# Kernel tuning notes

Measured on AMD Instinct MI355X. Metric: run time of the kernel, lower is better.

## Reference

```python
import jax, jax.numpy as jnp
import numpy as np

D, H, B = 16, 1024, 2048  # input_size, hidden_size, batch
EPS = 1e-12


def _masks():
    # MADE degree assignment, order 'A' (natural order)
    deg_in = jnp.arange(1, D + 1)                # [D]
    deg_h = jnp.arange(H) % (D - 1) + 1          # [H]
    m0 = (deg_h[:, None] >= deg_in[None, :]).astype(jnp.float32)  # [H, D] input->hidden
    m1 = (deg_h[:, None] >= deg_h[None, :]).astype(jnp.float32)   # [H, H] hidden->hidden
    m2 = (deg_in[:, None] > deg_h[None, :]).astype(jnp.float32)   # [D, H] hidden->output
    return m0, m1, m2


def setup_inputs() -> dict:
    key = jax.random.key(0)
    ks = jax.random.split(key, 8)

    def lin(k, out_d, in_d):
        k1, k2, k3 = jax.random.split(k, 3)
        v = jax.random.normal(k1, (out_d, in_d), jnp.float32)
        g = jax.random.uniform(k2, (out_d,), jnp.float32, 0.1, 0.2)  # small gain keeps logstd stable over D iters
        b = jax.random.normal(k3, (out_d,), jnp.float32) * 0.01
        return v, g, b

    inp = {"x": jax.random.normal(ks[0], (B, D), jnp.float32)}
    dims = [(H, D), (H, H), (D, H)]
    i = 1
    for n in ("mu", "lv"):
        for j, (o, ii) in enumerate(dims):
            v, g, b = lin(ks[i], o, ii)
            i += 1
            inp[f"{n}_v{j}"] = v
            inp[f"{n}_g{j}"] = g
            inp[f"{n}_b{j}"] = b
    return inp


def _wn(v, g, m):
    # weight-normalized masked linear weight: mask * g * v / ||v||
    return m * (g[:, None] * v / jnp.linalg.norm(v, axis=1, keepdims=True))


def _made(y, p):
    (w0, b0), (w1, b1), (w2, b2) = p
    h = jax.nn.elu(y @ w0.T + b0)   # [B, H]
    h = jax.nn.elu(h @ w1.T + b1)   # [B, H]
    return h @ w2.T + b2            # [B, D]


def reference(x, mu_v0, mu_g0, mu_b0, mu_v1, mu_g1, mu_b1, mu_v2, mu_g2, mu_b2,
              lv_v0, lv_g0, lv_b0, lv_v1, lv_g1, lv_b1, lv_v2, lv_g2, lv_b2):
    m0, m1, m2 = _masks()
    pm = ((_wn(mu_v0, mu_g0, m0), mu_b0), (_wn(mu_v1, mu_g1, m1), mu_b1), (_wn(mu_v2, mu_g2, m2), mu_b2))
    pl = ((_wn(lv_v0, lv_g0, m0), lv_b0), (_wn(lv_v1, lv_g1, m1), lv_b1), (_wn(lv_v2, lv_g2, m2), lv_b2))

    def step(carry, _):
        y, _ls = carry
        mu = _made(y, pm)
        logstd = _made(y, pl) * 0.5
        y_new = (x - mu) / (jnp.exp(logstd) + EPS)
        return (y_new, logstd), None

    init = (jnp.zeros_like(x), jnp.zeros_like(x))
    (y, logstd), _ = jax.lax.scan(step, init, None, length=D)
    return y, logstd.sum(axis=1)
```

## Files before the change

kernel.cpp:

```cpp
#include <hip/hip_runtime.h>
#include <cstdint>
#include <cstddef>


#define Dd 16
#define Hh 1024
#define Bb 2048
#define EPSV 1e-12f

typedef unsigned short u16;
typedef __attribute__((ext_vector_type(4))) float f32x4;
typedef __attribute__((ext_vector_type(8))) short s16x8;
typedef __attribute__((ext_vector_type(4))) u16 u16x4;
typedef __attribute__((ext_vector_type(8))) u16 u16x8;

__device__ __forceinline__ u16 f2bf(float f) {
  union { float f; unsigned u; } v; v.f = f;
  unsigned u = v.u;
  unsigned r = (u + 0x7fffu + ((u >> 16) & 1u)) >> 16;
  return (u16)r;
}
__device__ __forceinline__ float elu(float a) {
  return a > 0.f ? a : __expf(a) - 1.f;
}
__device__ __forceinline__ void barrier_lds() {
  asm volatile("s_waitcnt lgkmcnt(0)" ::: "memory");
  __builtin_amdgcn_s_barrier();
}

__device__ __forceinline__ int p_of(int i) {
  if (i < 276) { int g = i / 69, q = i - g * 69; return g + 15 * q; }
  int r = i - 276; int g = 4 + r / 68, q = r - (g - 4) * 68;
  return g + 15 * q;
}
__device__ __forceinline__ int g_of(int i) {
  return (i < 276) ? (i / 69) : (4 + (i - 276) / 68);
}
__device__ __forceinline__ int lb_of(int g) {
  return (g <= 4) ? 69 * g : 276 + 68 * (g - 4);
}
__device__ __forceinline__ int sz_of(int g) { return (g < 4) ? 69 : 68; }

#define W1P_NET (15 * 80 * 1024)
#define W2P_NET (15 * 16 * 104)
#define W0P_NET (15 * 80 * 32)

__global__ __launch_bounds__(256) void prep_all(
    const float* __restrict__ mu_v0, const float* __restrict__ mu_g0,
    const float* __restrict__ mu_b0,
    const float* __restrict__ mu_v1, const float* __restrict__ mu_g1,
    const float* __restrict__ mu_b1,
    const float* __restrict__ mu_v2, const float* __restrict__ mu_g2,
    const float* __restrict__ lv_v0, const float* __restrict__ lv_g0,
    const float* __restrict__ lv_b0,
    const float* __restrict__ lv_v1, const float* __restrict__ lv_g1,
    const float* __restrict__ lv_b1,
    const float* __restrict__ lv_v2, const float* __restrict__ lv_g2,
    u16* __restrict__ W1p, u16* __restrict__ W2p, u16* __restrict__ W0p,
    float* __restrict__ b1p, float* __restrict__ b0p) {
  int bid = blockIdx.x, tid = threadIdx.x;
  int l = tid & 63, w = tid >> 6;

  {
    int wid = bid * 4 + w;
    int net = wid / 1200, rem = wid % 1200;
    int g = rem / 80, u = rem % 80;
    u16* o = W1p + (size_t)wid * 1024;
    if (u < sz_of(g)) {
      int j = p_of(lb_of(g) + u);
      const float* v = (net ? lv_v1 : mu_v1) + (size_t)j * Hh;
      float val[4][4]; float ss = 0.f;
      for (int ii = 0; ii < 4; ++ii)
        for (int t = 0; t < 4; ++t) {
          int kp = ii * 256 + 4 * l + t;
          float xx = v[p_of(kp)];
          val[ii][t] = xx; ss += xx * xx;
        }
      for (int s = 32; s; s >>= 1) ss += __shfl_xor(ss, s);
      float sc = ((net ? lv_g1 : mu_g1)[j]) * rsqrtf(ss);
      for (int ii = 0; ii < 4; ++ii) {
        int k0 = ii * 256 + 4 * l;
        u16x4 wv;
        for (int t = 0; t < 4; ++t)
          wv[t] = f2bf((g >= g_of(k0 + t)) ? sc * val[ii][t] : 0.f);
        *(u16x4*)(o + k0) = wv;
      }
    } else {
      u16x4 z = {0, 0, 0, 0};
      for (int ii = 0; ii < 4; ++ii) *(u16x4*)(o + ii * 256 + 4 * l) = z;
    }
  }

  if (bid < 8) {
    int wid2 = bid * 4 + w;
    int nn = wid2 >> 4, oi = wid2 & 15;
    const float* v = (nn ? lv_v2 : mu_v2) + (size_t)oi * Hh;
    float ss = 0.f;
    for (int ii = 0; ii < 4; ++ii) {
      f32x4 vv = *(const f32x4*)(v + ii * 256 + 4 * l);
      ss += vv[0]*vv[0] + vv[1]*vv[1] + vv[2]*vv[2] + vv[3]*vv[3];
    }
    for (int s = 32; s; s >>= 1) ss += __shfl_xor(ss, s);
    float sc = ((nn ? lv_g2 : mu_g2)[oi]) * rsqrtf(ss);
    for (int e = l; e < 15 * 104; e += 64) {
      int g = e / 104, u = e % 104;
      float val = 0.f;
      if (u < sz_of(g) && oi > g) val = sc * v[p_of(lb_of(g) + u)];
      W2p[nn * W2P_NET + g * (16 * 104) + oi * 104 + u] = f2bf(val);
    }
  }

  if (bid >= 8 && bid < 18) {
    int idx = (bid - 8) * 256 + tid;
    if (idx < 2400) {
      int nn = idx / 1200, rem = idx % 1200;
      int g = rem / 80, u = rem % 80;
      u16* orow = W0p + nn * W0P_NET + g * (80 * 32) + u * 32;
      if (u < sz_of(g)) {
        int j = p_of(lb_of(g) + u);
        const float* v = (nn ? lv_v0 : mu_v0) + j * Dd;
        float vv[16]; float ss = 0.f;
        for (int k = 0; k < 16; ++k) { vv[k] = v[k]; ss += vv[k] * vv[k]; }
        float sc = ((nn ? lv_g0 : mu_g0)[j]) * rsqrtf(ss);
        for (int k = 0; k < 16; ++k)
          orow[k] = f2bf((g >= k) ? sc * vv[k] : 0.f);
        for (int k = 16; k < 32; ++k) orow[k] = 0;
        b0p[nn * 1200 + g * 80 + u] = (nn ? lv_b0 : mu_b0)[j];
        b1p[nn * 1200 + g * 80 + u] = (nn ? lv_b1 : mu_b1)[j];
      } else {
        for (int k = 0; k < 32; ++k) orow[k] = 0;
        b0p[nn * 1200 + g * 80 + u] = 0.f;
        b1p[nn * 1200 + g * 80 + u] = 0.f;
      }
    }
  }
}

__global__ __launch_bounds__(256) void prep_w1f(
    const u16* __restrict__ W1p, u16* __restrict__ W1f) {
  int t = blockIdx.x * 4 + (threadIdx.x >> 6);
  int l = threadIdx.x & 63;
  int net = t / 240, rem = t % 240;
  int g = rem >> 4, kt = rem & 15;
  if (kt >= ((lb_of(g + 1) + 63) >> 6)) return;
  const u16* src = W1p + (size_t)(net * 1200 + g * 80) * 1024;
  u16* dst = W1f + ((size_t)((net * 15 + g) * 16 + kt) * 10) * 512;
  for (int nf = 0; nf < 5; ++nf)
    for (int kk = 0; kk < 2; ++kk) {
      int u = nf * 16 + (l & 15);
      int k = kt * 64 + kk * 32 + ((l >> 4) << 3);
      u16x8 v = *(const u16x8*)(src + (size_t)u * 1024 + k);
      *(u16x8*)(dst + (size_t)(nf * 2 + kk) * 512 + l * 8) = v;
    }
}

#define LOADF(DST, BASE, KT)                                                \
  {                                                                         \
    const u16* fp_ = (BASE) + (size_t)(KT) * 5120;                          \
    _Pragma("unroll") for (int nf_ = 0; nf_ < 5; ++nf_)                     \
      _Pragma("unroll") for (int kk_ = 0; kk_ < 2; ++kk_)                   \
        DST[nf_][kk_] = *(const s16x8*)(fp_ + (nf_ * 2 + kk_) * 512);       \
  }
#define MFMAI(SLOT, KT)                                                     \
  {                                                                         \
    s16x8 a0_ = *(const s16x8*)(&h0L[net][lr][(KT) * 64 + lk * 8]);         \
    s16x8 a1_ = *(const s16x8*)(&h0L[net][lr][(KT) * 64 + 32 + lk * 8]);    \
    _Pragma("unroll") for (int nf_ = 0; nf_ < 5; ++nf_) {                   \
      hacc[nf_] = __builtin_amdgcn_mfma_f32_16x16x32_bf16(                  \
          a0_, SLOT[nf_][0], hacc[nf_], 0, 0, 0);                           \
      hacc[nf_] = __builtin_amdgcn_mfma_f32_16x16x32_bf16(                  \
          a1_, SLOT[nf_][1], hacc[nf_], 0, 0, 0);                           \
    }                                                                       \
  }

__global__ __launch_bounds__(512, 1) void afmade_main(
    const u16* __restrict__ W1f, const u16* __restrict__ W2p,
    const u16* __restrict__ W0p,
    const float* __restrict__ b1p, const float* __restrict__ b0p,
    const float* __restrict__ b2_mu, const float* __restrict__ b2_lv,
    const float* __restrict__ x, float* __restrict__ out) {
  __shared__ u16 h0L[2][16][1040];
  __shared__ float sPart[2][4][16][80];
  __shared__ u16 sH1[2][16][104];
  __shared__ u16 yb[16][40];
  __shared__ float sX[16][16];
  __shared__ float sB1L[2400];
  __shared__ float sB0L[2400];
  __shared__ float sB2[2][16];
  __shared__ float sLsum[16];

  const int tid = threadIdx.x;
  const int l = tid & 63, w = tid >> 6;
  const int net = w >> 2, kq = w & 3;
  const int lr = l & 15, lk = l >> 4;
  const int b0g = blockIdx.x * 16;

  {
    u16x8 z = {0, 0, 0, 0, 0, 0, 0, 0};
    for (int e = tid; e < 4160; e += 512) ((u16x8*)h0L)[e] = z;
    for (int e = tid; e < 416; e += 512) ((u16x8*)sH1)[e] = z;
    for (int e = tid; e < 80; e += 512) ((u16x8*)yb)[e] = z;
  }
  for (int e = tid; e < 256; e += 512)
    sX[e >> 4][e & 15] = x[(size_t)(b0g + (e >> 4)) * 16 + (e & 15)];
  for (int e = tid; e < 2400; e += 512) { sB1L[e] = b1p[e]; sB0L[e] = b0p[e]; }
  if (tid < 16) sB2[0][tid] = b2_mu[tid];
  else if (tid < 32) sB2[1][tid - 16] = b2_lv[tid - 16];
  else if (tid < 48) sLsum[tid - 32] = 0.f;
  f32x4 mlacc0 = {0.f, 0.f, 0.f, 0.f};
  f32x4 mlacc1 = {0.f, 0.f, 0.f, 0.f};

  s16x8 bfA[5][2], bfB[5][2], bfC[5][2];
  {
    const u16* base1 = W1f + ((size_t)((net * 15 + 0) * 16) * 10) * 512 +
                       (size_t)l * 8;
    if (kq < 2) LOADF(bfA, base1, kq);
  }
  __syncthreads();

  for (int s = 0; s < 16; ++s) {
    s16x8 w0pre0, w0pre1;
    if (s < 15) {
      const u16* W0g = W0p + net * W0P_NET + s * (80 * 32);
      w0pre0 = *(const s16x8*)(W0g + (kq * 16 + lr) * 32 + lk * 8);
      if (kq == 0)
        w0pre1 = *(const s16x8*)(W0g + (64 + lr) * 32 + lk * 8);
    }

    if (s > 0) {
      const int g = s - 1;
      const int ktn = (lb_of(s) + 63) >> 6;
      const int ktnN = (s < 15) ? ((lb_of(s + 1) + 63) >> 6) : 0;
      const u16* baseg = W1f + ((size_t)((net * 15 + g) * 16) * 10) * 512 +
                         (size_t)l * 8;
      const u16* basen = W1f + ((size_t)((net * 15 + s) * 16) * 10) * 512 +
                         (size_t)l * 8;
      s16x8 w2f[6];
      if (w == 0) {
#pragma unroll
        for (int c = 0; c < 3; ++c) {
          w2f[c] = *(const s16x8*)(W2p + g * (16 * 104) + lr * 104 +
                                   c * 32 + lk * 8);
          w2f[3 + c] = *(const s16x8*)(W2p + W2P_NET + g * (16 * 104) +
                                       lr * 104 + c * 32 + lk * 8);
        }
      }
      f32x4 hacc[5] = {};
      if (kq + 8 < ktn)  LOADF(bfC, baseg, kq + 8);
      if (kq < ktn)      MFMAI(bfA, kq);
      if (kq + 12 < ktn) LOADF(bfA, baseg, kq + 12);
      if (kq + 4 < ktn)  MFMAI(bfB, kq + 4);
      if (kq + 8 < ktn)  MFMAI(bfC, kq + 8);
      if (kq + 12 < ktn) MFMAI(bfA, kq + 12);
#pragma unroll
      for (int nf = 0; nf < 5; ++nf)
#pragma unroll
        for (int reg = 0; reg < 4; ++reg)
          sPart[net][kq][lk * 4 + reg][nf * 16 + lr] = hacc[nf][reg];
      if (s < 15) {
        if (kq < ktnN)     LOADF(bfA, basen, kq);
        if (kq + 4 < ktnN) LOADF(bfB, basen, kq + 4);
      }
      barrier_lds();
      {
        const int nn = tid >> 8;
        const int rr = (tid >> 4) & 15;
        const int u0 = tid & 15;
#pragma unroll
        for (int c = 0; c < 5; ++c) {
          int uu = c * 16 + u0;
          float v = sPart[nn][0][rr][uu] + sPart[nn][1][rr][uu] +
                    sPart[nn][2][rr][uu] + sPart[nn][3][rr][uu] +
                    sB1L[nn * 1200 + g * 80 + uu];
          sH1[nn][rr][uu] = f2bf(elu(v));
        }
      }
      barrier_lds();
      if (w == 0) {
#pragma unroll
        for (int c = 0; c < 3; ++c) {
          s16x8 a0 = *(const s16x8*)(&sH1[0][lr][c * 32 + lk * 8]);
          mlacc0 = __builtin_amdgcn_mfma_f32_16x16x32_bf16(
              a0, w2f[c], mlacc0, 0, 0, 0);
          s16x8 a1v = *(const s16x8*)(&sH1[1][lr][c * 32 + lk * 8]);
          mlacc1 = __builtin_amdgcn_mfma_f32_16x16x32_bf16(
              a1v, w2f[3 + c], mlacc1, 0, 0, 0);
        }
      }
    }
    if (w == 0 && lr == s) {
#pragma unroll
      for (int reg = 0; reg < 4; ++reg) {
        int r = lk * 4 + reg;
        float mu = mlacc0[reg] + sB2[0][s];
        float lv = mlacc1[reg] + sB2[1][s];
        float ls = 0.5f * lv;
        float yv = (sX[r][s] - mu) / (__expf(ls) + EPSV);
        out[(size_t)(b0g + r) * 16 + s] = yv;
        yb[r][s] = f2bf(yv);
        float ns = sLsum[r] + ls;
        sLsum[r] = ns;
        if (s == 15) out[Bb * 16 + b0g + r] = ns;
      }
    }
    barrier_lds();
    if (s < 15) {
      const int LbS = lb_of(s), szS = sz_of(s);
      s16x8 yfrag = *(const s16x8*)(&yb[lr][lk * 8]);
      {
        int nf = kq;
        int unit = nf * 16 + lr;
        f32x4 h = __builtin_amdgcn_mfma_f32_16x16x32_bf16(
            yfrag, w0pre0, (f32x4){0.f, 0.f, 0.f, 0.f}, 0, 0, 0);
        if (unit < szS) {
          float bias = sB0L[net * 1200 + s * 80 + unit];
#pragma unroll
          for (int reg = 0; reg < 4; ++reg)
            h0L[net][lk * 4 + reg][LbS + unit] = f2bf(elu(h[reg] + bias));
        }
      }
      if (kq == 0) {
        int unit = 64 + lr;
        f32x4 h = __builtin_amdgcn_mfma_f32_16x16x32_bf16(
            yfrag, w0pre1, (f32x4){0.f, 0.f, 0.f, 0.f}, 0, 0, 0);
        if (unit < szS) {
          float bias = sB0L[net * 1200 + s * 80 + unit];
#pragma unroll
          for (int reg = 0; reg < 4; ++reg)
            h0L[net][lk * 4 + reg][LbS + unit] = f2bf(elu(h[reg] + bias));
        }
      }
      barrier_lds();
    }
  }
}


extern "C" void kernel_launch(void* const* d_in, const int* in_sizes, int n_in,
                              void* d_out, int out_size, void* d_ws, size_t ws_size,
                              hipStream_t stream) {
  const float* x     = (const float*)d_in[0];
  const float* mu_v0 = (const float*)d_in[1];
  const float* mu_g0 = (const float*)d_in[2];
  const float* mu_b0 = (const float*)d_in[3];
  const float* mu_v1 = (const float*)d_in[4];
  const float* mu_g1 = (const float*)d_in[5];
  const float* mu_b1 = (const float*)d_in[6];
  const float* mu_v2 = (const float*)d_in[7];
  const float* mu_g2 = (const float*)d_in[8];
  const float* mu_b2 = (const float*)d_in[9];
  const float* lv_v0 = (const float*)d_in[10];
  const float* lv_g0 = (const float*)d_in[11];
  const float* lv_b0 = (const float*)d_in[12];
  const float* lv_v1 = (const float*)d_in[13];
  const float* lv_g1 = (const float*)d_in[14];
  const float* lv_b1 = (const float*)d_in[15];
  const float* lv_v2 = (const float*)d_in[16];
  const float* lv_g2 = (const float*)d_in[17];
  const float* lv_b2 = (const float*)d_in[18];

  char* ws = (char*)d_ws;
  u16*   W1p = (u16*)(ws);
  u16*   W2p = (u16*)(ws + 4915200);
  u16*   W0p = (u16*)(ws + 5015040);
  float* b1p = (float*)(ws + 5168640);
  float* b0p = (float*)(ws + 5178240);
  u16*   W1f = (u16*)(ws + 5187840);

  prep_all<<<600, 256, 0, stream>>>(
      mu_v0, mu_g0, mu_b0, mu_v1, mu_g1, mu_b1, mu_v2, mu_g2,
      lv_v0, lv_g0, lv_b0, lv_v1, lv_g1, lv_b1, lv_v2, lv_g2,
      W1p, W2p, W0p, b1p, b0p);
  prep_w1f<<<120, 256, 0, stream>>>(W1p, W1f);

  afmade_main<<<128, 512, 0, stream>>>(W1f, W2p, W0p, b1p, b0p,
                                       mu_b2, lv_b2, x, (float*)d_out);
}
```

Before: 81.43 us.

## Split batch into 8-row blocks of 4 waves to double grid size

Each block now handles 8 batch rows with 256 threads (2 waves per net splitting K) instead of 16 rows with 512 threads, and the grid goes from 128 to 256 blocks so more of the 256 CUs are used. The K-loop of the hidden-to-hidden MFMA is re-pipelined with two register buffers over 8 k-tiles per wave, and the partial-sum reduction drops from 4 to 2 slices. The 16-row MFMA tiles are now half wasted (rows duplicated via lr&7 and masked on store), and each block re-reads the full W1 weights, doubling global/L2 weight traffic.

```diff
diff --git a/kernel.cpp b/kernel.cpp
--- a/kernel.cpp
+++ b/kernel.cpp
@@ -163,8 +163,8 @@
   }
 #define MFMAI(SLOT, KT)                                                     \
   {                                                                         \
-    s16x8 a0_ = *(const s16x8*)(&h0L[net][lr][(KT) * 64 + lk * 8]);         \
-    s16x8 a1_ = *(const s16x8*)(&h0L[net][lr][(KT) * 64 + 32 + lk * 8]);    \
+    s16x8 a0_ = *(const s16x8*)(&h0L[net][lr & 7][(KT) * 64 + lk * 8]);     \
+    s16x8 a1_ = *(const s16x8*)(&h0L[net][lr & 7][(KT) * 64 + 32 + lk * 8]);\
     _Pragma("unroll") for (int nf_ = 0; nf_ < 5; ++nf_) {                   \
       hacc[nf_] = __builtin_amdgcn_mfma_f32_16x16x32_bf16(                  \
           a0_, SLOT[nf_][0], hacc[nf_], 0, 0, 0);                           \
@@ -173,44 +173,45 @@
     }                                                                       \
   }
 
-__global__ __launch_bounds__(512, 1) void afmade_main(
+__global__ __launch_bounds__(256, 2) void afmade_main(
     const u16* __restrict__ W1f, const u16* __restrict__ W2p,
     const u16* __restrict__ W0p,
     const float* __restrict__ b1p, const float* __restrict__ b0p,
     const float* __restrict__ b2_mu, const float* __restrict__ b2_lv,
     const float* __restrict__ x, float* __restrict__ out) {
-  __shared__ u16 h0L[2][16][1040];
-  __shared__ float sPart[2][4][16][80];
-  __shared__ u16 sH1[2][16][104];
-  __shared__ u16 yb[16][40];
-  __shared__ float sX[16][16];
+  __shared__ u16 h0L[2][8][1040];
+  __shared__ float sPart[2][2][8][80];
+  __shared__ u16 sH1[2][8][104];
+  __shared__ u16 yb[8][40];
+  __shared__ float sX[8][16];
   __shared__ float sB1L[2400];
   __shared__ float sB0L[2400];
   __shared__ float sB2[2][16];
-  __shared__ float sLsum[16];
+  __shared__ float sMLex[2][16];
+  __shared__ float sLsum[8];
 
   const int tid = threadIdx.x;
   const int l = tid & 63, w = tid >> 6;
-  const int net = w >> 2, kq = w & 3;
+  const int net = w >> 1, kq = w & 1;
   const int lr = l & 15, lk = l >> 4;
-  const int b0g = blockIdx.x * 16;
+  const int b0g = blockIdx.x * 8;
 
   {
     u16x8 z = {0, 0, 0, 0, 0, 0, 0, 0};
-    for (int e = tid; e < 4160; e += 512) ((u16x8*)h0L)[e] = z;
-    for (int e = tid; e < 416; e += 512) ((u16x8*)sH1)[e] = z;
-    for (int e = tid; e < 80; e += 512) ((u16x8*)yb)[e] = z;
-  }
-  for (int e = tid; e < 256; e += 512)
-    sX[e >> 4][e & 15] = x[(size_t)(b0g + (e >> 4)) * 16 + (e & 15)];
-  for (int e = tid; e < 2400; e += 512) { sB1L[e] = b1p[e]; sB0L[e] = b0p[e]; }
+    for (int e = tid; e < 2080; e += 256) ((u16x8*)h0L)[e] = z;
+    for (int e = tid; e < 208; e += 256) ((u16x8*)sH1)[e] = z;
+    if (tid < 40) ((u16x8*)yb)[tid] = z;
+  }
+  if (tid < 128) sX[tid >> 4][tid & 15] =
+      x[(size_t)(b0g + (tid >> 4)) * 16 + (tid & 15)];
+  for (int e = tid; e < 2400; e += 256) { sB1L[e] = b1p[e]; sB0L[e] = b0p[e]; }
   if (tid < 16) sB2[0][tid] = b2_mu[tid];
   else if (tid < 32) sB2[1][tid - 16] = b2_lv[tid - 16];
-  else if (tid < 48) sLsum[tid - 32] = 0.f;
+  else if (tid < 40) sLsum[tid - 32] = 0.f;
   f32x4 mlacc0 = {0.f, 0.f, 0.f, 0.f};
   f32x4 mlacc1 = {0.f, 0.f, 0.f, 0.f};
 
-  s16x8 bfA[5][2], bfB[5][2], bfC[5][2];
+  s16x8 bfA[5][2], bfB[5][2];
   {
     const u16* base1 = W1f + ((size_t)((net * 15 + 0) * 16) * 10) * 512 +
                        (size_t)l * 8;
@@ -219,12 +220,13 @@
   __syncthreads();
 
   for (int s = 0; s < 16; ++s) {
-    s16x8 w0pre0, w0pre1;
+    s16x8 w0pre0, w0pre1, w0pre2;
     if (s < 15) {
       const u16* W0g = W0p + net * W0P_NET + s * (80 * 32);
       w0pre0 = *(const s16x8*)(W0g + (kq * 16 + lr) * 32 + lk * 8);
+      w0pre1 = *(const s16x8*)(W0g + ((kq + 2) * 16 + lr) * 32 + lk * 8);
       if (kq == 0)
-        w0pre1 = *(const s16x8*)(W0g + (64 + lr) * 32 + lk * 8);
+        w0pre2 = *(const s16x8*)(W0g + (64 + lr) * 32 + lk * 8);
     }
 
     if (s > 0) {
@@ -246,31 +248,38 @@
         }
       }
       f32x4 hacc[5] = {};
-      if (kq + 8 < ktn)  LOADF(bfC, baseg, kq + 8);
+      if (kq + 2 < ktn)  LOADF(bfB, baseg, kq + 2);
       if (kq < ktn)      MFMAI(bfA, kq);
+      if (kq + 4 < ktn)  LOADF(bfA, baseg, kq + 4);
+      if (kq + 2 < ktn)  MFMAI(bfB, kq + 2);
+      if (kq + 6 < ktn)  LOADF(bfB, baseg, kq + 6);
+      if (kq + 4 < ktn)  MFMAI(bfA, kq + 4);
+      if (kq + 8 < ktn)  LOADF(bfA, baseg, kq + 8);
+      if (kq + 6 < ktn)  MFMAI(bfB, kq + 6);
+      if (kq + 10 < ktn) LOADF(bfB, baseg, kq + 10);
+      if (kq + 8 < ktn)  MFMAI(bfA, kq + 8);
       if (kq + 12 < ktn) LOADF(bfA, baseg, kq + 12);
-      if (kq + 4 < ktn)  MFMAI(bfB, kq + 4);
-      if (kq + 8 < ktn)  MFMAI(bfC, kq + 8);
+      if (kq + 10 < ktn) MFMAI(bfB, kq + 10);
+      if (kq + 14 < ktn) LOADF(bfB, baseg, kq + 14);
       if (kq + 12 < ktn) MFMAI(bfA, kq + 12);
+      if (kq + 14 < ktn) MFMAI(bfB, kq + 14);
 #pragma unroll
       for (int nf = 0; nf < 5; ++nf)
 #pragma unroll
-        for (int reg = 0; reg < 4; ++reg)
-          sPart[net][kq][lk * 4 + reg][nf * 16 + lr] = hacc[nf][reg];
-      if (s < 15) {
-        if (kq < ktnN)     LOADF(bfA, basen, kq);
-        if (kq + 4 < ktnN) LOADF(bfB, basen, kq + 4);
-      }
+        for (int reg = 0; reg < 4; ++reg) {
+          int row = lk * 4 + reg;
+          if (row < 8) sPart[net][kq][row][nf * 16 + lr] = hacc[nf][reg];
+        }
+      if (s < 15 && kq < ktnN) LOADF(bfA, basen, kq);
       barrier_lds();
       {
-        const int nn = tid >> 8;
-        const int rr = (tid >> 4) & 15;
+        const int nn = tid >> 7;
+        const int rr = (tid >> 4) & 7;
         const int u0 = tid & 15;
 #pragma unroll
         for (int c = 0; c < 5; ++c) {
           int uu = c * 16 + u0;
           float v = sPart[nn][0][rr][uu] + sPart[nn][1][rr][uu] +
-                    sPart[nn][2][rr][uu] + sPart[nn][3][rr][uu] +
                     sB1L[nn * 1200 + g * 80 + uu];
           sH1[nn][rr][uu] = f2bf(elu(v));
         }
@@ -279,10 +288,10 @@
       if (w == 0) {
 #pragma unroll
         for (int c = 0; c < 3; ++c) {
-          s16x8 a0 = *(const s16x8*)(&sH1[0][lr][c * 32 + lk * 8]);
+          s16x8 a0 = *(const s16x8*)(&sH1[0][lr & 7][c * 32 + lk * 8]);
           mlacc0 = __builtin_amdgcn_mfma_f32_16x16x32_bf16(
               a0, w2f[c], mlacc0, 0, 0, 0);
-          s16x8 a1v = *(const s16x8*)(&sH1[1][lr][c * 32 + lk * 8]);
+          s16x8 a1v = *(const s16x8*)(&sH1[1][lr & 7][c * 32 + lk * 8]);
           mlacc1 = __builtin_amdgcn_mfma_f32_16x16x32_bf16(
               a1v, w2f[3 + c], mlacc1, 0, 0, 0);
         }
@@ -292,42 +301,60 @@
 #pragma unroll
       for (int reg = 0; reg < 4; ++reg) {
         int r = lk * 4 + reg;
-        float mu = mlacc0[reg] + sB2[0][s];
-        float lv = mlacc1[reg] + sB2[1][s];
-        float ls = 0.5f * lv;
-        float yv = (sX[r][s] - mu) / (__expf(ls) + EPSV);
-        out[(size_t)(b0g + r) * 16 + s] = yv;
-        yb[r][s] = f2bf(yv);
-        float ns = sLsum[r] + ls;
-        sLsum[r] = ns;
-        if (s == 15) out[Bb * 16 + b0g + r] = ns;
+        if (r < 8) {
+          float mu = mlacc0[reg] + sB2[0][s];
+          float lv = mlacc1[reg] + sB2[1][s];
+          float ls = 0.5f * lv;
+          float yv = (sX[r][s] - mu) / (__expf(ls) + EPSV);
+          out[(size_t)(b0g + r) * 16 + s] = yv;
+          yb[r][s] = f2bf(yv);
+          float ns = sLsum[r] + ls;
+          sLsum[r] = ns;
+          if (s == 15) out[Bb * 16 + b0g + r] = ns;
+        }
       }
     }
     barrier_lds();
     if (s < 15) {
       const int LbS = lb_of(s), szS = sz_of(s);
-      s16x8 yfrag = *(const s16x8*)(&yb[lr][lk * 8]);
+      s16x8 yfrag = *(const s16x8*)(&yb[lr & 7][lk * 8]);
       {
-        int nf = kq;
-        int unit = nf * 16 + lr;
+        int unit = kq * 16 + lr;
         f32x4 h = __builtin_amdgcn_mfma_f32_16x16x32_bf16(
             yfrag, w0pre0, (f32x4){0.f, 0.f, 0.f, 0.f}, 0, 0, 0);
         if (unit < szS) {
           float bias = sB0L[net * 1200 + s * 80 + unit];
 #pragma unroll
-          for (int reg = 0; reg < 4; ++reg)
-            h0L[net][lk * 4 + reg][LbS + unit] = f2bf(elu(h[reg] + bias));
-        }
-      }
-      if (kq == 0) {
-        int unit = 64 + lr;
+          for (int reg = 0; reg < 4; ++reg) {
+            int row = lk * 4 + reg;
+            if (row < 8) h0L[net][row][LbS + unit] = f2bf(elu(h[reg] + bias));
+          }
+        }
+      }
+      {
+        int unit = (kq + 2) * 16 + lr;
         f32x4 h = __builtin_amdgcn_mfma_f32_16x16x32_bf16(
             yfrag, w0pre1, (f32x4){0.f, 0.f, 0.f, 0.f}, 0, 0, 0);
         if (unit < szS) {
           float bias = sB0L[net * 1200 + s * 80 + unit];
 #pragma unroll
-          for (int reg = 0; reg < 4; ++reg)
-            h0L[net][lk * 4 + reg][LbS + unit] = f2bf(elu(h[reg] + bias));
+          for (int reg = 0; reg < 4; ++reg) {
+            int row = lk * 4 + reg;
+            if (row < 8) h0L[net][row][LbS + unit] = f2bf(elu(h[reg] + bias));
+          }
+        }
+      }
+      if (kq == 0) {
+        int unit = 64 + lr;
+        f32x4 h = __builtin_amdgcn_mfma_f32_16x16x32_bf16(
+            yfrag, w0pre2, (f32x4){0.f, 0.f, 0.f, 0.f}, 0, 0, 0);
+        if (unit < szS) {
+          float bias = sB0L[net * 1200 + s * 80 + unit];
+#pragma unroll
+          for (int reg = 0; reg < 4; ++reg) {
+            int row = lk * 4 + reg;
+            if (row < 8) h0L[net][row][LbS + unit] = f2bf(elu(h[reg] + bias));
+          }
         }
       }
       barrier_lds();
@@ -373,6 +400,6 @@
       W1p, W2p, W0p, b1p, b0p);
   prep_w1f<<<120, 256, 0, stream>>>(W1p, W1f);
 
-  afmade_main<<<128, 512, 0, stream>>>(W1f, W2p, W0p, b1p, b0p,
+  afmade_main<<<256, 256, 0, stream>>>(W1f, W2p, W0p, b1p, b0p,
                                        mu_b2, lv_b2, x, (float*)d_out);
 }
```

Measured after the change: 94.66 us. 1.16x slower.

## Fuse W1 fragment packing into prep and cut register buffers in main loop

Applied to the files above, without the earlier changes.

The prep kernel now writes W1 weights directly in the MFMA fragment layout and fills b1p itself, which removes the separate prep_w1f launch and the intermediate W1p buffer. In the main kernel, the W1 prefetch pipeline drops from three register buffers to two with reordered load/MFMA interleaving. Every wave now redundantly computes the small output MFMAs and y values, so a full block barrier can be replaced by a local lgkmcnt wait. This lowers register pressure and launch overhead, at the cost of less prefetch depth, redundant work across waves, and scattered writes during prep.

```diff
diff --git a/kernel.cpp b/kernel.cpp
--- a/kernel.cpp
+++ b/kernel.cpp
@@ -41,7 +41,6 @@
 }
 __device__ __forceinline__ int sz_of(int g) { return (g < 4) ? 69 : 68; }
 
-#define W1P_NET (15 * 80 * 1024)
 #define W2P_NET (15 * 16 * 104)
 #define W0P_NET (15 * 80 * 32)
 
@@ -56,7 +55,7 @@
     const float* __restrict__ lv_v1, const float* __restrict__ lv_g1,
     const float* __restrict__ lv_b1,
     const float* __restrict__ lv_v2, const float* __restrict__ lv_g2,
-    u16* __restrict__ W1p, u16* __restrict__ W2p, u16* __restrict__ W0p,
+    u16* __restrict__ W1f, u16* __restrict__ W2p, u16* __restrict__ W0p,
     float* __restrict__ b1p, float* __restrict__ b0p) {
   int bid = blockIdx.x, tid = threadIdx.x;
   int l = tid & 63, w = tid >> 6;
@@ -65,7 +64,8 @@
     int wid = bid * 4 + w;
     int net = wid / 1200, rem = wid % 1200;
     int g = rem / 80, u = rem % 80;
-    u16* o = W1p + (size_t)wid * 1024;
+    u16* dstb = W1f + ((size_t)((net * 15 + g) * 16) * 10) * 512;
+    const int nf = u >> 4, lane16 = u & 15;
     if (u < sz_of(g)) {
       int j = p_of(lb_of(g) + u);
       const float* v = (net ? lv_v1 : mu_v1) + (size_t)j * Hh;
@@ -83,11 +83,22 @@
         u16x4 wv;
         for (int t = 0; t < 4; ++t)
           wv[t] = f2bf((g >= g_of(k0 + t)) ? sc * val[ii][t] : 0.f);
-        *(u16x4*)(o + k0) = wv;
-      }
+        int kt = k0 >> 6, kk = (k0 >> 5) & 1;
+        int lanep = lane16 + 16 * ((k0 & 31) >> 3);
+        *(u16x4*)(dstb + (size_t)(kt * 10 + nf * 2 + kk) * 512 +
+                  lanep * 8 + (k0 & 7)) = wv;
+      }
+      if (l == 0) b1p[wid] = (net ? lv_b1 : mu_b1)[j];
     } else {
       u16x4 z = {0, 0, 0, 0};
-      for (int ii = 0; ii < 4; ++ii) *(u16x4*)(o + ii * 256 + 4 * l) = z;
+      for (int ii = 0; ii < 4; ++ii) {
+        int k0 = ii * 256 + 4 * l;
+        int kt = k0 >> 6, kk = (k0 >> 5) & 1;
+        int lanep = lane16 + 16 * ((k0 & 31) >> 3);
+        *(u16x4*)(dstb + (size_t)(kt * 10 + nf * 2 + kk) * 512 +
+                  lanep * 8 + (k0 & 7)) = z;
+      }
+      if (l == 0) b1p[wid] = 0.f;
     }
   }
 
@@ -126,32 +137,12 @@
           orow[k] = f2bf((g >= k) ? sc * vv[k] : 0.f);
         for (int k = 16; k < 32; ++k) orow[k] = 0;
         b0p[nn * 1200 + g * 80 + u] = (nn ? lv_b0 : mu_b0)[j];
-        b1p[nn * 1200 + g * 80 + u] = (nn ? lv_b1 : mu_b1)[j];
       } else {
         for (int k = 0; k < 32; ++k) orow[k] = 0;
         b0p[nn * 1200 + g * 80 + u] = 0.f;
-        b1p[nn * 1200 + g * 80 + u] = 0.f;
-      }
-    }
-  }
-}
-
-__global__ __launch_bounds__(256) void prep_w1f(
-    const u16* __restrict__ W1p, u16* __restrict__ W1f) {
-  int t = blockIdx.x * 4 + (threadIdx.x >> 6);
-  int l = threadIdx.x & 63;
-  int net = t / 240, rem = t % 240;
-  int g = rem >> 4, kt = rem & 15;
-  if (kt >= ((lb_of(g + 1) + 63) >> 6)) return;
-  const u16* src = W1p + (size_t)(net * 1200 + g * 80) * 1024;
-  u16* dst = W1f + ((size_t)((net * 15 + g) * 16 + kt) * 10) * 512;
-  for (int nf = 0; nf < 5; ++nf)
-    for (int kk = 0; kk < 2; ++kk) {
-      int u = nf * 16 + (l & 15);
-      int k = kt * 64 + kk * 32 + ((l >> 4) << 3);
-      u16x8 v = *(const u16x8*)(src + (size_t)u * 1024 + k);
-      *(u16x8*)(dst + (size_t)(nf * 2 + kk) * 512 + l * 8) = v;
-    }
+      }
+    }
+  }
 }
 
 #define LOADF(DST, BASE, KT)                                                \
@@ -210,7 +201,7 @@
   f32x4 mlacc0 = {0.f, 0.f, 0.f, 0.f};
   f32x4 mlacc1 = {0.f, 0.f, 0.f, 0.f};
 
-  s16x8 bfA[5][2], bfB[5][2], bfC[5][2];
+  s16x8 bfA[5][2], bfB[5][2];
   {
     const u16* base1 = W1f + ((size_t)((net * 15 + 0) * 16) * 10) * 512 +
                        (size_t)l * 8;
@@ -236,31 +227,27 @@
       const u16* basen = W1f + ((size_t)((net * 15 + s) * 16) * 10) * 512 +
                          (size_t)l * 8;
       s16x8 w2f[6];
-      if (w == 0) {
-#pragma unroll
-        for (int c = 0; c < 3; ++c) {
-          w2f[c] = *(const s16x8*)(W2p + g * (16 * 104) + lr * 104 +
-                                   c * 32 + lk * 8);
-          w2f[3 + c] = *(const s16x8*)(W2p + W2P_NET + g * (16 * 104) +
-                                       lr * 104 + c * 32 + lk * 8);
-        }
+#pragma unroll
+      for (int c = 0; c < 3; ++c) {
+        w2f[c] = *(const s16x8*)(W2p + g * (16 * 104) + lr * 104 +
+                                 c * 32 + lk * 8);
+        w2f[3 + c] = *(const s16x8*)(W2p + W2P_NET + g * (16 * 104) +
+                                     lr * 104 + c * 32 + lk * 8);
       }
       f32x4 hacc[5] = {};
-      if (kq + 8 < ktn)  LOADF(bfC, baseg, kq + 8);
+      if (kq + 4 < ktn)  LOADF(bfB, baseg, kq + 4);
       if (kq < ktn)      MFMAI(bfA, kq);
-      if (kq + 12 < ktn) LOADF(bfA, baseg, kq + 12);
+      if (kq + 8 < ktn)  LOADF(bfA, baseg, kq + 8);
       if (kq + 4 < ktn)  MFMAI(bfB, kq + 4);
-      if (kq + 8 < ktn)  MFMAI(bfC, kq + 8);
-      if (kq + 12 < ktn) MFMAI(bfA, kq + 12);
+      if (kq + 12 < ktn) LOADF(bfB, baseg, kq + 12);
+      if (kq + 8 < ktn)  MFMAI(bfA, kq + 8);
+      if (kq + 12 < ktn) MFMAI(bfB, kq + 12);
 #pragma unroll
       for (int nf = 0; nf < 5; ++nf)
 #pragma unroll
         for (int reg = 0; reg < 4; ++reg)
           sPart[net][kq][lk * 4 + reg][nf * 16 + lr] = hacc[nf][reg];
-      if (s < 15) {
-        if (kq < ktnN)     LOADF(bfA, basen, kq);
-        if (kq + 4 < ktnN) LOADF(bfB, basen, kq + 4);
-      }
+      if (s < 15 && kq < ktnN) LOADF(bfA, basen, kq);
       barrier_lds();
       {
         const int nn = tid >> 8;
@@ -276,19 +263,17 @@
         }
       }
       barrier_lds();
-      if (w == 0) {
-#pragma unroll
-        for (int c = 0; c < 3; ++c) {
-          s16x8 a0 = *(const s16x8*)(&sH1[0][lr][c * 32 + lk * 8]);
-          mlacc0 = __builtin_amdgcn_mfma_f32_16x16x32_bf16(
-              a0, w2f[c], mlacc0, 0, 0, 0);
-          s16x8 a1v = *(const s16x8*)(&sH1[1][lr][c * 32 + lk * 8]);
-          mlacc1 = __builtin_amdgcn_mfma_f32_16x16x32_bf16(
-              a1v, w2f[3 + c], mlacc1, 0, 0, 0);
-        }
-      }
-    }
-    if (w == 0 && lr == s) {
+#pragma unroll
+      for (int c = 0; c < 3; ++c) {
+        s16x8 a0 = *(const s16x8*)(&sH1[0][lr][c * 32 + lk * 8]);
+        mlacc0 = __builtin_amdgcn_mfma_f32_16x16x32_bf16(
+            a0, w2f[c], mlacc0, 0, 0, 0);
+        s16x8 a1v = *(const s16x8*)(&sH1[1][lr][c * 32 + lk * 8]);
+        mlacc1 = __builtin_amdgcn_mfma_f32_16x16x32_bf16(
+            a1v, w2f[3 + c], mlacc1, 0, 0, 0);
+      }
+    }
+    if (lr == s) {
 #pragma unroll
       for (int reg = 0; reg < 4; ++reg) {
         int r = lk * 4 + reg;
@@ -296,20 +281,21 @@
         float lv = mlacc1[reg] + sB2[1][s];
         float ls = 0.5f * lv;
         float yv = (sX[r][s] - mu) / (__expf(ls) + EPSV);
-        out[(size_t)(b0g + r) * 16 + s] = yv;
         yb[r][s] = f2bf(yv);
-        float ns = sLsum[r] + ls;
-        sLsum[r] = ns;
-        if (s == 15) out[Bb * 16 + b0g + r] = ns;
-      }
-    }
-    barrier_lds();
+        if (w == 0) {
+          out[(size_t)(b0g + r) * 16 + s] = yv;
+          float ns = sLsum[r] + ls;
+          sLsum[r] = ns;
+          if (s == 15) out[Bb * 16 + b0g + r] = ns;
+        }
+      }
+    }
+    asm volatile("s_waitcnt lgkmcnt(0)" ::: "memory");
     if (s < 15) {
       const int LbS = lb_of(s), szS = sz_of(s);
       s16x8 yfrag = *(const s16x8*)(&yb[lr][lk * 8]);
       {
-        int nf = kq;
-        int unit = nf * 16 + lr;
+        int unit = kq * 16 + lr;
         f32x4 h = __builtin_amdgcn_mfma_f32_16x16x32_bf16(
             yfrag, w0pre0, (f32x4){0.f, 0.f, 0.f, 0.f}, 0, 0, 0);
         if (unit < szS) {
@@ -360,18 +346,16 @@
   const float* lv_b2 = (const float*)d_in[18];
 
   char* ws = (char*)d_ws;
-  u16*   W1p = (u16*)(ws);
+  u16*   W1f = (u16*)(ws);
   u16*   W2p = (u16*)(ws + 4915200);
   u16*   W0p = (u16*)(ws + 5015040);
   float* b1p = (float*)(ws + 5168640);
   float* b0p = (float*)(ws + 5178240);
-  u16*   W1f = (u16*)(ws + 5187840);
 
   prep_all<<<600, 256, 0, stream>>>(
       mu_v0, mu_g0, mu_b0, mu_v1, mu_g1, mu_b1, mu_v2, mu_g2,
       lv_v0, lv_g0, lv_b0, lv_v1, lv_g1, lv_b1, lv_v2, lv_g2,
-      W1p, W2p, W0p, b1p, b0p);
-  prep_w1f<<<120, 256, 0, stream>>>(W1p, W1f);
+      W1f, W2p, W0p, b1p, b0p);
 
   afmade_main<<<128, 512, 0, stream>>>(W1f, W2p, W0p, b1p, b0p,
                                        mu_b2, lv_b2, x, (float*)d_out);
```

After: 76.24 us. -6.4%, faster.
